# Kernel tuning notes

Hardware: AMD Instinct MI355X
Metric: run time of the kernel (lower is better)

## Reference

```python
import jax, jax.numpy as jnp
import numpy as np

BT, C, H, W = 16, 64, 128, 128
K, S = 16, 8            # ksize, stride2
MID = C // 2            # BasicBlock mid channels
INTER = C // 1          # r = 1 -> inter_channels = channels
NH = (H - K) // S + 1
NW = (W - K) // S + 1
L = NH * NW             # 225 patches


def _lrelu(x):
    return jnp.where(x > 0, x, 0.2 * x)


def _conv(x, w):
    return jax.lax.conv_general_dilated(
        x, w, window_strides=(1, 1), padding='VALID',
        dimension_numbers=('NCHW', 'OIHW', 'NCHW'))


def setup_inputs() -> dict:
    key = jax.random.key(0)
    ks = jax.random.split(key, 7)
    fea = jax.random.normal(ks[0], (BT, C, H, W), jnp.float32)
    spa_graph = jax.random.normal(ks[1], (BT, L, L), jnp.float32) * 0.05
    spe_graph = jax.random.normal(ks[2], (BT, C, C), jnp.float32) * 0.05
    W1 = jax.random.normal(ks[3], (MID, C, 3, 3), jnp.float32) * 0.05
    W2 = jax.random.normal(ks[4], (C, MID, 1, 1), jnp.float32) * 0.05
    Wl = jax.random.normal(ks[5], (INTER, C, 1, 1), jnp.float32) * 0.05
    bl = jnp.zeros((INTER,), jnp.float32)
    return {'fea': fea, 'spa_graph': spa_graph, 'spe_graph': spe_graph,
            'W1': W1, 'W2': W2, 'Wl': Wl, 'bl': bl}


def reference(fea, spa_graph, spe_graph, W1, W2, Wl, bl):
    bt, c, h, w = fea.shape
    # BasicBlock: reflect-pad conv3x3 -> lrelu -> conv1x1 -> lrelu
    xp = jnp.pad(fea, ((0, 0), (0, 0), (1, 1), (1, 1)), mode='reflect')
    f = _lrelu(_conv(_lrelu(_conv(xp, W1)), W2))            # [bt,c,h,w]

    # unfold (torch.nn.Unfold order: (C, kh, kw) feature-major, row-major patches)
    patches = jax.lax.conv_general_dilated_patches(f, (K, K), (S, S), 'VALID')
    cols = patches.reshape(bt, c * K * K, L)                 # [bt,F,L]

    # per-sample spatial-graph matmul: graph[p,q] @ patches[q,F]
    out_spa = jnp.einsum('bpq,bfq->bfp', spa_graph, cols)    # [bt,F,L]

    # fold: overlap-add patches back to [bt,c,h,w]
    rows = jnp.arange(NH) * S + jnp.arange(K)[:, None]       # [K,NH]
    colsi = jnp.arange(NW) * S + jnp.arange(K)[:, None]      # [K,NW]
    lin = (rows[:, None, :, None] * w + colsi[None, :, None, :]).reshape(-1)
    vals = out_spa.reshape(bt, c, K * K * L)
    x = jnp.zeros((bt, c, h * w), fea.dtype).at[:, :, lin].add(vals)
    x = x.reshape(bt, c, h, w)

    # per-sample spectral-graph matmul
    residual = jnp.einsum('bcd,bdn->bcn', spe_graph,
                          f.reshape(bt, c, h * w)).reshape(bt, c, h, w)

    xa = 0.5 * (x + residual)
    xl = _lrelu(_conv(xa, Wl) + bl[None, :, None, None])
    wei = jax.nn.sigmoid(xl)
    return x * wei + residual * (1.0 - wei) + f
```

## Files before the change

### kernel.cpp

```cpp
#include <hip/hip_runtime.h>
#include <hip/hip_bf16.h>
#include <hip/hip_runtime_api.h>

#define BT 16
#define CCH 64
#define H 128
#define W 128
#define STR 8
#define NH 15
#define NW 15
#define L 225
#define HW (H * W)

#define UPITCH 264
#define RP 72
#define CP 72
#define MP 40

typedef __attribute__((ext_vector_type(8))) short short8;
typedef __attribute__((ext_vector_type(4))) float f32x4;
typedef __attribute__((ext_vector_type(4))) unsigned short ushort4_t;

__device__ __forceinline__ float lrelu(float v) { return v > 0.f ? v : 0.2f * v; }
__device__ __forceinline__ unsigned short f2bf(float v) {
  __hip_bfloat16 h = __float2bfloat16(v);
  unsigned short u;
  __builtin_memcpy(&u, &h, 2);
  return u;
}
__device__ __forceinline__ float bf2f(unsigned short u) {
  unsigned int x = ((unsigned int)u) << 16;
  float f;
  __builtin_memcpy(&f, &x, 4);
  return f;
}

__global__ __launch_bounds__(256) void prep_all_k(
    const float* __restrict__ spa, const float* __restrict__ W1,
    const float* __restrict__ W2, const float* __restrict__ spe,
    const float* __restrict__ Wl, __hip_bfloat16* __restrict__ T,
    __hip_bfloat16* __restrict__ W1r, __hip_bfloat16* __restrict__ W2r,
    __hip_bfloat16* __restrict__ spe_r, __hip_bfloat16* __restrict__ wl_r) {
  const int bid = blockIdx.x;
  const int tid = threadIdx.x;

  if (bid < 4096) {
    const int bp = bid;
    const int b = bp >> 8, pi = bp & 255;
    const int k = tid;
    const int yi = pi >> 4, xi = pi & 15;
    const int ky = k >> 4, kx = k & 15;
    const float* sb = spa + (size_t)b * L * L;
    float acc = 0.f;
#pragma unroll
    for (int vy = 0; vy < 2; ++vy)
#pragma unroll
      for (int vx = 0; vx < 2; ++vx) {
        const int py = yi - vy, px = xi - vx;
        const int qy = ky - vy, qx = kx - vx;
        if (py >= 0 && py < NH && px >= 0 && px < NW && qy >= 0 && qy < NH &&
            qx >= 0 && qx < NW)
          acc += sb[(py * NW + px) * L + qy * NW + qx];
      }
    T[(size_t)bp * 256 + k] = __float2bfloat16(acc);
    return;
  }

  const int idx = (bid - 4096) * 256 + tid;
  if (idx < 18432) {
    const int kk = idx >> 10, mc = (idx >> 5) & 31, ck = idx & 31;
    const int pos = kk >> 1, s = kk & 1;
    W1r[idx] = __float2bfloat16(W1[(mc * 64 + s * 32 + ck) * 9 + pos]);
    return;
  }
  int i = idx - 18432;
  if (i < 2048) { W2r[i] = __float2bfloat16(W2[i]); return; }
  i -= 2048;
  if (i < BT * CCH * CCH) { spe_r[i] = __float2bfloat16(spe[i]); return; }
  i -= BT * CCH * CCH;
  if (i < CCH * CCH) { wl_r[i] = __float2bfloat16(Wl[i]); return; }
}

__global__ __launch_bounds__(512) void bblock_mfma_k(
    const float* __restrict__ fea, const __hip_bfloat16* __restrict__ W1r,
    const __hip_bfloat16* __restrict__ W2r, __hip_bfloat16* __restrict__ fnh) {
  __shared__ __align__(16) short sbuf[324 * CP];
  short* st = sbuf;
  short* mids = sbuf;
  unsigned short* fst = (unsigned short*)sbuf;

  const int lb = ((int)blockIdx.x % 8) * 128 + (int)blockIdx.x / 8;
  const int b = lb >> 6;
  const int tile = lb & 63;
  const int ty0 = (tile >> 3) * 16, tx0 = (tile & 7) * 16;
  const int tid = threadIdx.x;

  const int qbase = tx0 - 4;
  for (int i = tid; i < 64 * 108; i += 512) {
    const int c = i & 63;
    const int r = i >> 6;
    const int iy = r / 6, q = r - iy * 6;
    const int gq = qbase + q * 4;
    int gy = ty0 + iy - 1;
    gy = gy < 0 ? -gy : (gy > 127 ? 254 - gy : gy);
    if (gq >= 0 && gq <= 124) {
      const f32x4 v =
          *(const f32x4*)&fea[((size_t)(b * CCH + c) * H + gy) * W + gq];
#pragma unroll
      for (int j = 0; j < 4; ++j) {
        const int ix = q * 4 + j - 3;
        if (ix >= 0 && ix < 18)
          st[(iy * 18 + ix) * CP + c] = (short)f2bf(v[j]);
      }
    }
  }
  if (tx0 == 0) {
    __syncthreads();
    for (int i = tid; i < 64 * 18; i += 512) {
      const int c = i & 63, iy = i >> 6;
      st[(iy * 18 + 0) * CP + c] = st[(iy * 18 + 2) * CP + c];
    }
  } else if (tx0 == 112) {
    __syncthreads();
    for (int i = tid; i < 64 * 18; i += 512) {
      const int c = i & 63, iy = i >> 6;
      st[(iy * 18 + 17) * CP + c] = st[(iy * 18 + 15) * CP + c];
    }
  }
  __syncthreads();

  const int w = tid >> 6, lane = tid & 63, lm = lane & 15, lk = lane >> 4;
  const short* w1 = (const short*)W1r;
  const short* w2 = (const short*)W2r;

  f32x4 acc[2][2];
#pragma unroll
  for (int mt = 0; mt < 2; ++mt)
#pragma unroll
    for (int t = 0; t < 2; ++t) acc[mt][t] = (f32x4){0.f, 0.f, 0.f, 0.f};

#pragma unroll
  for (int pos = 0; pos < 9; ++pos) {
    const int dy = pos / 3, dx = pos - dy * 3;
#pragma unroll
    for (int s = 0; s < 2; ++s) {
      short8 a0 = *(const short8*)&w1[((pos * 2 + s) * 32 + lm) * 32 + lk * 8];
      short8 a1 = *(const short8*)&w1[((pos * 2 + s) * 32 + 16 + lm) * 32 + lk * 8];
#pragma unroll
      for (int t = 0; t < 2; ++t) {
        const int p = (w * 2 + t + dy) * 18 + lm + dx;
        short8 bb = *(const short8*)&st[p * CP + s * 32 + lk * 8];
        acc[0][t] = __builtin_amdgcn_mfma_f32_16x16x32_bf16(a0, bb, acc[0][t], 0, 0, 0);
        acc[1][t] = __builtin_amdgcn_mfma_f32_16x16x32_bf16(a1, bb, acc[1][t], 0, 0, 0);
      }
    }
  }

  __syncthreads();

#pragma unroll
  for (int t = 0; t < 2; ++t) {
    const int n = (w * 2 + t) * 16 + lm;
#pragma unroll
    for (int mt = 0; mt < 2; ++mt) {
      ushort4_t pk;
#pragma unroll
      for (int r = 0; r < 4; ++r) pk[r] = f2bf(lrelu(acc[mt][t][r]));
      *(ushort4_t*)&mids[n * MP + mt * 16 + lk * 4] = pk;
    }
  }
  __syncthreads();

  f32x4 acc2[4][2];
#pragma unroll
  for (int m2 = 0; m2 < 4; ++m2)
#pragma unroll
    for (int t = 0; t < 2; ++t) acc2[m2][t] = (f32x4){0.f, 0.f, 0.f, 0.f};

  short8 b2[2];
#pragma unroll
  for (int t = 0; t < 2; ++t)
    b2[t] = *(const short8*)&mids[((w * 2 + t) * 16 + lm) * MP + lk * 8];
#pragma unroll
  for (int m2 = 0; m2 < 4; ++m2) {
    short8 a2 = *(const short8*)&w2[(m2 * 16 + lm) * 32 + lk * 8];
#pragma unroll
    for (int t = 0; t < 2; ++t)
      acc2[m2][t] = __builtin_amdgcn_mfma_f32_16x16x32_bf16(a2, b2[t], acc2[m2][t], 0, 0, 0);
  }

  __syncthreads();

#pragma unroll
  for (int m2 = 0; m2 < 4; ++m2)
#pragma unroll
    for (int t = 0; t < 2; ++t) {
      ushort4_t pk;
#pragma unroll
      for (int r = 0; r < 4; ++r) pk[r] = f2bf(lrelu(acc2[m2][t][r]));
      *(ushort4_t*)&fst[((w * 2 + t) * 16 + lm) * RP + m2 * 16 + lk * 4] = pk;
    }
  __syncthreads();

  unsigned short* fo = (unsigned short*)fnh;
  for (int i = tid; i < 2048; i += 512) {
    const int lp = i >> 3, g = i & 7;
    const int y = ty0 + (lp >> 4), x = tx0 + (lp & 15);
    *(short8*)&fo[((size_t)b * HW + y * W + x) * CCH + g * 8] =
        *(const short8*)&fst[lp * RP + g * 8];
  }
}

__global__ __launch_bounds__(512) void spa_mfma_k(
    const __hip_bfloat16* __restrict__ fnh, const __hip_bfloat16* __restrict__ T,
    __hip_bfloat16* __restrict__ xnh) {
  __shared__ __align__(16) short us[256 * RP];

  const int lb = ((int)blockIdx.x % 8) * 128 + (int)blockIdx.x / 8;
  const int b = lb >> 6, ky0 = (lb >> 3) & 7, kx0 = lb & 7;
  const int tid = threadIdx.x;

  const unsigned short* fb = (const unsigned short*)fnh + (size_t)b * HW * CCH;

  for (int i = tid; i < 2048; i += 512) {
    const int pos = i >> 3, g = i & 7;
    const int gy = pos >> 4, gx = pos & 15;
    const int blk = pos >> 3;
    short8 v = *(const short8*)&fb[((ky0 + 8 * gy) * W + kx0 + 8 * gx) * CCH + g * 8];
#pragma unroll
    for (int e = 0; e < 8; ++e) {
      const int c = g * 8 + e;
      const int sblk = (blk & ~7) | ((blk ^ (c >> 3)) & 7);
      us[c * UPITCH + sblk * 8 + (pos & 7)] = v[e];
    }
  }
  __syncthreads();

  const int w = tid >> 6, lane = tid & 63;
  const int lm = lane & 15, lk = lane >> 4;
  const int mtg = w >> 2, ntg = w & 3;

  const short* tb = (const short*)T + (size_t)b * 256 * 256;

  f32x4 acc[2][4];
#pragma unroll
  for (int mt = 0; mt < 2; ++mt)
#pragma unroll
    for (int n = 0; n < 4; ++n) acc[mt][n] = (f32x4){0.f, 0.f, 0.f, 0.f};

  const int c0 = (mtg * 2) * 16 + lm, c1 = (mtg * 2 + 1) * 16 + lm;

#pragma unroll
  for (int k8 = 0; k8 < 8; ++k8) {
    const int kb = k8 * 4 + lk;
    const int sb0 = (kb & ~7) | ((kb ^ (c0 >> 3)) & 7);
    const int sb1 = (kb & ~7) | ((kb ^ (c1 >> 3)) & 7);
    short8 a0 = *(const short8*)&us[c0 * UPITCH + sb0 * 8];
    short8 a1 = *(const short8*)&us[c1 * UPITCH + sb1 * 8];
    short8 bb[4];
#pragma unroll
    for (int n = 0; n < 4; ++n)
      bb[n] = *(const short8*)&tb[((ntg * 4 + n) * 16 + lm) * 256 + k8 * 32 + lk * 8];
#pragma unroll
    for (int n = 0; n < 4; ++n) {
      acc[0][n] = __builtin_amdgcn_mfma_f32_16x16x32_bf16(a0, bb[n], acc[0][n], 0, 0, 0);
      acc[1][n] = __builtin_amdgcn_mfma_f32_16x16x32_bf16(a1, bb[n], acc[1][n], 0, 0, 0);
    }
  }

  __syncthreads();

  unsigned short* xst = (unsigned short*)us;
#pragma unroll
  for (int mt = 0; mt < 2; ++mt)
#pragma unroll
    for (int n = 0; n < 4; ++n) {
      ushort4_t pk;
#pragma unroll
      for (int r = 0; r < 4; ++r) pk[r] = f2bf(acc[mt][n][r]);
      *(ushort4_t*)&xst[((ntg * 4 + n) * 16 + lm) * RP + (mtg * 2 + mt) * 16 + lk * 4] = pk;
    }
  __syncthreads();

  unsigned short* xo = (unsigned short*)xnh + (size_t)b * HW * CCH;
  for (int i = tid; i < 2048; i += 512) {
    const int pi = i >> 3, g = i & 7;
    const int row = (pi >> 4) * 8 + ky0;
    const int col = (pi & 15) * 8 + kx0;
    *(short8*)&xo[((size_t)row * W + col) * CCH + g * 8] =
        *(const short8*)&xst[pi * RP + g * 8];
  }
}

__global__ __launch_bounds__(256) void final_mfma_k(
    const __hip_bfloat16* __restrict__ fnh, const __hip_bfloat16* __restrict__ xnh,
    const __hip_bfloat16* __restrict__ spe_r, const __hip_bfloat16* __restrict__ wl_r,
    const float* __restrict__ bl, float* __restrict__ xo) {
  __shared__ __align__(16) short fl[128 * CP];
  __shared__ __align__(16) short xbuf[128 * CP];
  const int lb = ((int)blockIdx.x % 8) * 256 + (int)blockIdx.x / 8;
  const int b = lb >> 7;
  const int px0 = (lb & 127) * 128;
  const int tid = threadIdx.x;

  const unsigned short* xg = (const unsigned short*)xnh + (size_t)b * HW * CCH;
  for (int i = tid; i < 128 * 8; i += 256) {
    const int px = i >> 3, g = i & 7;
    *(short8*)&fl[px * CP + g * 8] =
        *(const short8*)&fnh[((size_t)b * HW + px0 + px) * CCH + g * 8];
    *(short8*)&xbuf[px * CP + g * 8] =
        *(const short8*)&xg[(size_t)(px0 + px) * CCH + g * 8];
  }
  __syncthreads();

  const int w = tid >> 6, lane = tid & 63, lm = lane & 15, lk = lane >> 4;
  const int c0 = w * 16 + lk * 4;

  const short* sa = (const short*)spe_r + ((size_t)b * CCH + w * 16 + lm) * CCH;
  const short8 a1_0 = *(const short8*)&sa[lk * 8];
  const short8 a1_1 = *(const short8*)&sa[32 + lk * 8];

  unsigned short* xbu = (unsigned short*)xbuf;

  f32x4 res[8];
  f32x4 xar[8];
#pragma unroll
  for (int nt = 0; nt < 8; ++nt) {
    const int prow = (nt * 16 + lm) * CP;
    short8 b0 = *(const short8*)&fl[prow + lk * 8];
    short8 b1 = *(const short8*)&fl[prow + 32 + lk * 8];
    f32x4 r = (f32x4){0.f, 0.f, 0.f, 0.f};
    r = __builtin_amdgcn_mfma_f32_16x16x32_bf16(a1_0, b0, r, 0, 0, 0);
    r = __builtin_amdgcn_mfma_f32_16x16x32_bf16(a1_1, b1, r, 0, 0, 0);
    res[nt] = r;
    ushort4_t xq = *(const ushort4_t*)&xbu[prow + c0];
    ushort4_t pk;
    f32x4 xa;
#pragma unroll
    for (int j = 0; j < 4; ++j) {
      xa[j] = 0.5f * (bf2f(xq[j]) + r[j]);
      pk[j] = f2bf(xa[j]);
    }
    xar[nt] = xa;
    *(ushort4_t*)&xbu[prow + c0] = pk;
  }
  __syncthreads();

  const short* wa = (const short*)wl_r + (w * 16 + lm) * CCH;
  const short8 a2_0 = *(const short8*)&wa[lk * 8];
  const short8 a2_1 = *(const short8*)&wa[32 + lk * 8];
  float blv[4];
#pragma unroll
  for (int j = 0; j < 4; ++j) blv[j] = bl[c0 + j];

#pragma unroll
  for (int nt = 0; nt < 8; ++nt) {
    const int prow = (nt * 16 + lm) * CP;
    short8 b0 = *(const short8*)&xbuf[prow + lk * 8];
    short8 b1 = *(const short8*)&xbuf[prow + 32 + lk * 8];
    f32x4 t = (f32x4){0.f, 0.f, 0.f, 0.f};
    t = __builtin_amdgcn_mfma_f32_16x16x32_bf16(a2_0, b0, t, 0, 0, 0);
    t = __builtin_amdgcn_mfma_f32_16x16x32_bf16(a2_1, b1, t, 0, 0, 0);
    ushort4_t fpk = *(const ushort4_t*)&fl[prow + c0];
#pragma unroll
    for (int j = 0; j < 4; ++j) {
      const float xl = lrelu(t[j] + blv[j]);
      const float wei = 1.f / (1.f + __expf(-xl));
      const float o = 2.f * xar[nt][j] * wei + res[nt][j] * (1.f - 2.f * wei) +
                      bf2f(fpk[j]);
      xo[((size_t)b * CCH + c0 + j) * HW + px0 + nt * 16 + lm] = o;
    }
  }
}

extern "C" void kernel_launch(void* const* d_in, const int* in_sizes, int n_in,
                              void* d_out, int out_size, void* d_ws,
                              size_t ws_size, hipStream_t stream) {
  const float* fea = (const float*)d_in[0];
  const float* spa = (const float*)d_in[1];
  const float* spe = (const float*)d_in[2];
  const float* W1  = (const float*)d_in[3];
  const float* W2  = (const float*)d_in[4];
  const float* Wl  = (const float*)d_in[5];
  const float* bl  = (const float*)d_in[6];
  float* out = (float*)d_out;

  const size_t XNH_BYTES = (size_t)BT * HW * CCH * 2;
  const size_t FNH_BYTES = (size_t)BT * HW * CCH * 2;
  const size_t T_BYTES   = (size_t)BT * 256 * 256 * 2;
  char* wsb = (char*)d_ws;
  __hip_bfloat16* xnh = (__hip_bfloat16*)wsb;
  __hip_bfloat16* fnh = (__hip_bfloat16*)(wsb + XNH_BYTES);
  __hip_bfloat16* T   = (__hip_bfloat16*)(wsb + XNH_BYTES + FNH_BYTES);
  char* wtb = wsb + XNH_BYTES + FNH_BYTES + T_BYTES;
  __hip_bfloat16* W1r   = (__hip_bfloat16*)wtb;
  __hip_bfloat16* W2r   = (__hip_bfloat16*)(wtb + 36864);
  __hip_bfloat16* spe_r = (__hip_bfloat16*)(wtb + 36864 + 4096);
  __hip_bfloat16* wl_r  = (__hip_bfloat16*)(wtb + 36864 + 4096 + 131072);

  prep_all_k<<<dim3(4448), 256, 0, stream>>>(spa, W1, W2, spe, Wl,
                                             T, W1r, W2r, spe_r, wl_r);
  bblock_mfma_k<<<dim3(1024), 512, 0, stream>>>(fea, W1r, W2r, fnh);
  spa_mfma_k<<<dim3(BT * 64), 512, 0, stream>>>(fnh, T, xnh);
  final_mfma_k<<<dim3(2048), 256, 0, stream>>>(fnh, xnh, spe_r, wl_r, bl, out);
}
```

Before: 124.6 us.

## Fuse spatial-graph T construction into basic-block kernel and split weight packing

```diff
diff --git a/kernel.cpp b/kernel.cpp
--- a/kernel.cpp
+++ b/kernel.cpp
@@ -35,19 +35,38 @@
   return f;
 }
 
-__global__ __launch_bounds__(256) void prep_all_k(
-    const float* __restrict__ spa, const float* __restrict__ W1,
-    const float* __restrict__ W2, const float* __restrict__ spe,
-    const float* __restrict__ Wl, __hip_bfloat16* __restrict__ T,
+__global__ __launch_bounds__(256) void wpack_k(
+    const float* __restrict__ W1, const float* __restrict__ W2,
+    const float* __restrict__ spe, const float* __restrict__ Wl,
     __hip_bfloat16* __restrict__ W1r, __hip_bfloat16* __restrict__ W2r,
     __hip_bfloat16* __restrict__ spe_r, __hip_bfloat16* __restrict__ wl_r) {
+  const int idx = blockIdx.x * 256 + threadIdx.x;
+  if (idx < 18432) {
+    const int kk = idx >> 10, mc = (idx >> 5) & 31, ck = idx & 31;
+    const int pos = kk >> 1, s = kk & 1;
+    W1r[idx] = __float2bfloat16(W1[(mc * 64 + s * 32 + ck) * 9 + pos]);
+    return;
+  }
+  int i = idx - 18432;
+  if (i < 2048) { W2r[i] = __float2bfloat16(W2[i]); return; }
+  i -= 2048;
+  if (i < BT * CCH * CCH) { spe_r[i] = __float2bfloat16(spe[i]); return; }
+  i -= BT * CCH * CCH;
+  if (i < CCH * CCH) { wl_r[i] = __float2bfloat16(Wl[i]); return; }
+}
+
+__global__ __launch_bounds__(512) void bblock_T_k(
+    const float* __restrict__ fea, const float* __restrict__ spa,
+    const __hip_bfloat16* __restrict__ W1r, const __hip_bfloat16* __restrict__ W2r,
+    __hip_bfloat16* __restrict__ fnh, __hip_bfloat16* __restrict__ T) {
+  __shared__ __align__(16) short sbuf[324 * CP];
   const int bid = blockIdx.x;
   const int tid = threadIdx.x;
 
-  if (bid < 4096) {
-    const int bp = bid;
+  if (bid >= 1024) {
+    const int bp = ((bid - 1024) << 1) + (tid >> 8);
     const int b = bp >> 8, pi = bp & 255;
-    const int k = tid;
+    const int k = tid & 255;
     const int yi = pi >> 4, xi = pi & 15;
     const int ky = k >> 4, kx = k & 15;
     const float* sb = spa + (size_t)b * L * L;
@@ -66,39 +85,19 @@
     return;
   }
 
-  const int idx = (bid - 4096) * 256 + tid;
-  if (idx < 18432) {
-    const int kk = idx >> 10, mc = (idx >> 5) & 31, ck = idx & 31;
-    const int pos = kk >> 1, s = kk & 1;
-    W1r[idx] = __float2bfloat16(W1[(mc * 64 + s * 32 + ck) * 9 + pos]);
-    return;
-  }
-  int i = idx - 18432;
-  if (i < 2048) { W2r[i] = __float2bfloat16(W2[i]); return; }
-  i -= 2048;
-  if (i < BT * CCH * CCH) { spe_r[i] = __float2bfloat16(spe[i]); return; }
-  i -= BT * CCH * CCH;
-  if (i < CCH * CCH) { wl_r[i] = __float2bfloat16(Wl[i]); return; }
-}
-
-__global__ __launch_bounds__(512) void bblock_mfma_k(
-    const float* __restrict__ fea, const __hip_bfloat16* __restrict__ W1r,
-    const __hip_bfloat16* __restrict__ W2r, __hip_bfloat16* __restrict__ fnh) {
-  __shared__ __align__(16) short sbuf[324 * CP];
   short* st = sbuf;
   short* mids = sbuf;
   unsigned short* fst = (unsigned short*)sbuf;
 
-  const int lb = ((int)blockIdx.x % 8) * 128 + (int)blockIdx.x / 8;
+  const int lb = (bid % 8) * 128 + bid / 8;
   const int b = lb >> 6;
   const int tile = lb & 63;
   const int ty0 = (tile >> 3) * 16, tx0 = (tile & 7) * 16;
-  const int tid = threadIdx.x;
 
   const int qbase = tx0 - 4;
   for (int i = tid; i < 64 * 108; i += 512) {
-    const int c = i & 63;
-    const int r = i >> 6;
+    const int c = i / 108;
+    const int r = i - c * 108;
     const int iy = r / 6, q = r - iy * 6;
     const int gq = qbase + q * 4;
     int gy = ty0 + iy - 1;
@@ -398,9 +397,8 @@
   __hip_bfloat16* spe_r = (__hip_bfloat16*)(wtb + 36864 + 4096);
   __hip_bfloat16* wl_r  = (__hip_bfloat16*)(wtb + 36864 + 4096 + 131072);
 
-  prep_all_k<<<dim3(4448), 256, 0, stream>>>(spa, W1, W2, spe, Wl,
-                                             T, W1r, W2r, spe_r, wl_r);
-  bblock_mfma_k<<<dim3(1024), 512, 0, stream>>>(fea, W1r, W2r, fnh);
+  wpack_k<<<dim3(352), 256, 0, stream>>>(W1, W2, spe, Wl, W1r, W2r, spe_r, wl_r);
+  bblock_T_k<<<dim3(3072), 512, 0, stream>>>(fea, spa, W1r, W2r, fnh, T);
   spa_mfma_k<<<dim3(BT * 64), 512, 0, stream>>>(fnh, T, xnh);
   final_mfma_k<<<dim3(2048), 256, 0, stream>>>(fnh, xnh, spe_r, wl_r, bl, out);
 }
```

After: 121.1 us. 1.03x faster.
